# Performance work log

Measured on AMD Instinct MI355X. Metric: run time of the kernel, lower is better.

Reference implementation:

```python
import jax, jax.numpy as jnp
import numpy as np

B, IN, H = 131072, 128, 128


def setup_inputs() -> dict:
    key = jax.random.key(0)
    ks = jax.random.split(key, 8)
    scale_W = 1.0 / np.sqrt(IN + H)
    scale_r = 1.0 / np.sqrt(H)
    return {
        "x": jax.random.normal(ks[0], (B, IN), jnp.float32),
        "h": jax.random.normal(ks[1], (B, H), jnp.float32),
        "c": jax.random.normal(ks[2], (B, H), jnp.float32),
        "n": jax.random.uniform(ks[3], (B, H), jnp.float32, 0.1, 1.0),
        "m": jax.random.normal(ks[4], (B, H), jnp.float32),
        "W": jax.random.normal(ks[5], (IN + H, 4 * H), jnp.float32) * scale_W,
        "r": jax.random.normal(ks[6], (H, 4 * H), jnp.float32) * scale_r,
        "b": jnp.zeros((4 * H,), jnp.float32),
    }


def reference(x, h, c, n, m, W, r, b):
    # fused gate pre-activations: [B, 4H]
    combined = jnp.concatenate((x, h), axis=1)
    gates = combined @ W + h @ r + b
    i_raw, f_raw, z_raw, o_raw = jnp.split(gates, 4, axis=1)
    i = jnp.exp(i_raw)
    f = jax.nn.sigmoid(f_raw)
    z = jnp.tanh(z_raw)
    o = jax.nn.sigmoid(o_raw)
    # log-domain stabilizer (max trick), faithful to source incl. m overwrite
    m_new = jnp.maximum(jnp.log(f) + m, jnp.log(i))
    i_prime = jnp.exp(jnp.log(i) - m_new)
    f_prime = jnp.exp(jnp.log(f) + m_new - m_new)  # == f, as in source
    c_new = f_prime * c + i_prime * z
    n_new = f_prime * n + i_prime
    h_tilde = c_new / n_new
    h_new = o * jnp.tanh(h_tilde)
    return (h_new, c_new, n_new, m_new)
```

## Files before the change

kernel.cpp:

```cpp
#include <hip/hip_runtime.h>
#include <cstdint>

#define NROWS 131072
#define HD    128
#define NDIM  512
#define OUTQ  16777216

using bf16x8 = __attribute__((ext_vector_type(8))) short;
using f32x4  = __attribute__((ext_vector_type(4))) float;

#define SB() __builtin_amdgcn_sched_barrier(0)

__device__ __forceinline__ uint32_t bf16rne(float f) {
  uint32_t u = __builtin_bit_cast(uint32_t, f);
  return (u + 0x7fffu + ((u >> 16) & 1u)) >> 16;
}

__device__ __forceinline__ float tanhf_fast(float v) {
  float a = __builtin_fabsf(v);
  float e = __expf(-2.0f * a);
  float t = (1.0f - e) * __builtin_amdgcn_rcpf(1.0f + e);
  return v < 0.0f ? -t : t;
}

__device__ __forceinline__ f32x4 ldv(const float* p) {
  return *reinterpret_cast<const f32x4*>(p);
}

#define ASYNC16(g, l)                                                        \
  __builtin_amdgcn_global_load_lds(                                          \
      (const __attribute__((address_space(1))) void*)(g),                    \
      (__attribute__((address_space(3))) void*)(l), 16, 0, 0)

__global__ __launch_bounds__(256) void pack_weights(
    const float* __restrict__ W, const float* __restrict__ r,
    uint16_t* __restrict__ Bp) {
  int idx = blockIdx.x * 256 + threadIdx.x;
  int l  = idx & 63;
  int ts = idx >> 6;
  int s  = ts & 7;
  int t  = ts >> 3;
  int g  = t >> 3;
  int u  = t & 7;
  int t2 = u >> 1;
  int p  = u & 1;
  int m  = l & 15;
  int ncol  = g * 128 + t2 * 32 + ((m >> 2) << 3) + p * 4 + (m & 3);
  int kbase = s * 32 + ((l >> 4) << 3);
  uint32_t w[4];
#pragma unroll
  for (int jj = 0; jj < 4; ++jj) {
    int k0 = kbase + 2 * jj;
    float v0 = W[k0 * NDIM + ncol];
    float v1 = W[(k0 + 1) * NDIM + ncol];
    if (k0 >= 128)     v0 += r[(k0 - 128) * NDIM + ncol];
    if (k0 + 1 >= 128) v1 += r[(k0 + 1 - 128) * NDIM + ncol];
    w[jj] = bf16rne(v0) | (bf16rne(v1) << 16);
  }
  reinterpret_cast<uint4*>(Bp)[idx] = make_uint4(w[0], w[1], w[2], w[3]);
}

__global__ __launch_bounds__(256, 2) void slstm_fused(
    const float* __restrict__ x,  const float* __restrict__ h,
    const float* __restrict__ cs, const float* __restrict__ ns,
    const float* __restrict__ ms, const float* __restrict__ bias,
    const uint16_t* __restrict__ Bp, float* __restrict__ out) {
  __shared__ __align__(16) char smem[65536];
  const int tid  = threadIdx.x;
  const int wave = tid >> 6;
  const int lane = tid & 63;
  const int row0 = blockIdx.x * 64;
  const int l15  = lane & 15;
  const int lg   = lane >> 4;

  const int    myrow = row0 + wave * 16 + l15;
  const size_t rbase = (size_t)myrow * HD;
  const int    jb8   = lg * 8;
  const int    rl    = wave * 16 + l15;

  const char* wBytes = (const char*)Bp;
#define DMA_HALFSTEP(u)                                                      \
  {                                                                          \
    const char* gsrc = wBytes + (((size_t)(wave * 8 + (u)) * 8) << 10) + (lane << 4); \
    char* ldst = smem + (wave << 13);                                        \
    _Pragma("unroll")                                                        \
    for (int k = 0; k < 8; ++k)                                              \
      ASYNC16(gsrc + (k << 10), ldst + (k << 10));                           \
  }

  f32x4 cvA = ldv(cs + rbase + jb8), cvHiA = ldv(cs + rbase + jb8 + 4);
  f32x4 nvA = ldv(ns + rbase + jb8), nvHiA = ldv(ns + rbase + jb8 + 4);
  f32x4 mvA = ldv(ms + rbase + jb8), mvHiA = ldv(ms + rbase + jb8 + 4);

  DMA_HALFSTEP(0)

  bf16x8 a[8];
#pragma unroll
  for (int s = 0; s < 8; ++s) {
    const float* src = (s < 4 ? x : h) + rbase + ((s & 3) * 32 + lg * 8);
    f32x4 v0 = ldv(src);
    f32x4 v1 = ldv(src + 4);
    bf16x8 pk;
    pk[0] = (short)bf16rne(v0[0]);
    pk[1] = (short)bf16rne(v0[1]);
    pk[2] = (short)bf16rne(v0[2]);
    pk[3] = (short)bf16rne(v0[3]);
    pk[4] = (short)bf16rne(v1[0]);
    pk[5] = (short)bf16rne(v1[1]);
    pk[6] = (short)bf16rne(v1[2]);
    pk[7] = (short)bf16rne(v1[3]);
    a[s] = pk;
  }
  __syncthreads();

#define MFMA_PHASE(AI, AF, AZ, AO)                                           \
  {                                                                          \
    _Pragma("unroll")                                                        \
    for (int s = 0; s < 8; ++s) {                                            \
      const int lo = lane << 4;                                              \
      bf16x8 wI = *reinterpret_cast<const bf16x8*>(smem + ((0 * 8 + s) << 10) + lo); \
      bf16x8 wF = *reinterpret_cast<const bf16x8*>(smem + ((1 * 8 + s) << 10) + lo); \
      bf16x8 wZ = *reinterpret_cast<const bf16x8*>(smem + ((2 * 8 + s) << 10) + lo); \
      bf16x8 wO = *reinterpret_cast<const bf16x8*>(smem + ((3 * 8 + s) << 10) + lo); \
      AI = __builtin_amdgcn_mfma_f32_16x16x32_bf16(wI, a[s], AI, 0, 0, 0);   \
      AF = __builtin_amdgcn_mfma_f32_16x16x32_bf16(wF, a[s], AF, 0, 0, 0);   \
      AZ = __builtin_amdgcn_mfma_f32_16x16x32_bf16(wZ, a[s], AZ, 0, 0, 0);   \
      AO = __builtin_amdgcn_mfma_f32_16x16x32_bf16(wO, a[s], AO, 0, 0, 0);   \
    }                                                                        \
  }

  char* sbuf = smem + 32768;

#pragma unroll
  for (int t2 = 0; t2 < 4; ++t2) {
    const int cb = t2 * 32 + jb8;

    const f32x4 cvLo = cvA,   cvHi = cvHiA;
    const f32x4 nvLo = nvA,   nvHi = nvHiA;
    const f32x4 mvLo = mvA,   mvHi = mvHiA;

    SB(); asm volatile("s_waitcnt vmcnt(8)" ::: "memory"); SB();
    __builtin_amdgcn_s_barrier(); SB();

    f32x4 accI0 = {0,0,0,0}, accF0 = {0,0,0,0}, accZ0 = {0,0,0,0}, accO0 = {0,0,0,0};
    MFMA_PHASE(accI0, accF0, accZ0, accO0)

    SB(); __builtin_amdgcn_s_barrier(); SB();
    DMA_HALFSTEP(2 * t2 + 1)
    SB();
    asm volatile("s_waitcnt vmcnt(0)" ::: "memory"); SB();
    __builtin_amdgcn_s_barrier(); SB();

    const f32x4 bIlo = ldv(bias + cb),        bIhi = ldv(bias + cb + 4);
    const f32x4 bFlo = ldv(bias + 128 + cb),  bFhi = ldv(bias + 128 + cb + 4);
    const f32x4 bZlo = ldv(bias + 256 + cb),  bZhi = ldv(bias + 256 + cb + 4);
    const f32x4 bOlo = ldv(bias + 384 + cb),  bOhi = ldv(bias + 384 + cb + 4);
    if (t2 < 3) {
      const size_t pp = rbase + (t2 + 1) * 32 + jb8;
      cvA = ldv(cs + pp); cvHiA = ldv(cs + pp + 4);
      nvA = ldv(ns + pp); nvHiA = ldv(ns + pp + 4);
      mvA = ldv(ms + pp); mvHiA = ldv(ms + pp + 4);
    }

    f32x4 accI1 = {0,0,0,0}, accF1 = {0,0,0,0}, accZ1 = {0,0,0,0}, accO1 = {0,0,0,0};
    MFMA_PHASE(accI1, accF1, accZ1, accO1)

    f32x4 hnLo, hnHi, cnLo, cnHi, nnLo, nnHi, mnLo, mnHi;
#pragma unroll
    for (int d = 0; d < 8; ++d) {
      const int pp = d >> 2, rr = d & 3;
      const float i_raw = (pp ? accI1[rr] : accI0[rr]) + (pp ? bIhi[rr] : bIlo[rr]);
      const float f_raw = (pp ? accF1[rr] : accF0[rr]) + (pp ? bFhi[rr] : bFlo[rr]);
      const float z_raw = (pp ? accZ1[rr] : accZ0[rr]) + (pp ? bZhi[rr] : bZlo[rr]);
      const float o_raw = (pp ? accO1[rr] : accO0[rr]) + (pp ? bOhi[rr] : bOlo[rr]);
      const float cV = pp ? cvHi[rr] : cvLo[rr];
      const float nV = pp ? nvHi[rr] : nvLo[rr];
      const float mV = pp ? mvHi[rr] : mvLo[rr];
      float ef  = __expf(-f_raw);
      float den = 1.0f + ef;
      float fg  = __builtin_amdgcn_rcpf(den);
      float lgf = -__logf(den);
      float mnv = fmaxf(lgf + mV, i_raw);
      float ip  = __expf(i_raw - mnv);
      float zt  = tanhf_fast(z_raw);
      float og  = __builtin_amdgcn_rcpf(1.0f + __expf(-o_raw));
      float cnv = fg * cV + ip * zt;
      float nnv = fg * nV + ip;
      float hnv = og * tanhf_fast(cnv * __builtin_amdgcn_rcpf(nnv));
      if (pp == 0) { hnLo[rr] = hnv; cnLo[rr] = cnv; nnLo[rr] = nnv; mnLo[rr] = mnv; }
      else         { hnHi[rr] = hnv; cnHi[rr] = cnv; nnHi[rr] = nnv; mnHi[rr] = mnv; }
    }

    {
      const int rb   = rl << 7;
      const int sw   = rl & 7;
      const int kLo  = (lg << 1);
      const int kHi  = (lg << 1) | 1;
      const int oLo  = rb + (((kLo) ^ sw) << 4);
      const int oHi  = rb + (((kHi) ^ sw) << 4);
      *reinterpret_cast<f32x4*>(sbuf + 0 * 8192 + oLo) = hnLo;
      *reinterpret_cast<f32x4*>(sbuf + 0 * 8192 + oHi) = hnHi;
      *reinterpret_cast<f32x4*>(sbuf + 1 * 8192 + oLo) = cnLo;
      *reinterpret_cast<f32x4*>(sbuf + 1 * 8192 + oHi) = cnHi;
      *reinterpret_cast<f32x4*>(sbuf + 2 * 8192 + oLo) = nnLo;
      *reinterpret_cast<f32x4*>(sbuf + 2 * 8192 + oHi) = nnHi;
      *reinterpret_cast<f32x4*>(sbuf + 3 * 8192 + oLo) = mnLo;
      *reinterpret_cast<f32x4*>(sbuf + 3 * 8192 + oHi) = mnHi;
    }
    SB(); asm volatile("s_waitcnt lgkmcnt(0)" ::: "memory"); SB();
    __builtin_amdgcn_s_barrier(); SB();

    if (t2 < 3) DMA_HALFSTEP(2 * t2 + 2)
    SB();

    {
      float* abase = out + (size_t)wave * OUTQ + (size_t)row0 * HD + t2 * 32;
      const char* sb = sbuf + (wave << 13);
#pragma unroll
      for (int i = 0; i < 8; ++i) {
        const int r  = i * 8 + (lane >> 3);
        const int k  = lane & 7;
        f32x4 v = *reinterpret_cast<const f32x4*>(
            sb + (r << 7) + (((k ^ (r & 7))) << 4));
        __builtin_nontemporal_store(
            v, reinterpret_cast<f32x4*>(abase + (size_t)r * HD + k * 4));
      }
    }
  }
#undef DMA_HALFSTEP
#undef MFMA_PHASE
}

extern "C" void kernel_launch(void* const* d_in, const int* in_sizes, int n_in,
                              void* d_out, int out_size, void* d_ws, size_t ws_size,
                              hipStream_t stream) {
  const float* x = (const float*)d_in[0];
  const float* h = (const float*)d_in[1];
  const float* c = (const float*)d_in[2];
  const float* n = (const float*)d_in[3];
  const float* m = (const float*)d_in[4];
  const float* W = (const float*)d_in[5];
  const float* r = (const float*)d_in[6];
  const float* b = (const float*)d_in[7];
  uint16_t* Bp = (uint16_t*)d_ws;

  pack_weights<<<64, 256, 0, stream>>>(W, r, Bp);
  slstm_fused<<<NROWS / 64, 256, 0, stream>>>(x, h, c, n, m, b, Bp, (float*)d_out);
}
```

Baseline: 131.1 us.

## Double-buffer weight halves in LDS and split output staging into two passes

Weight tiles for both MFMA halves of a step are now prefetched together into two separate 32KB LDS regions. This removes the mid-step barrier and the DMA wait between the two MFMA phases. To fit in LDS, output staging is cut to 16KB and done in two rounds (h/c, then n/m), which adds barriers and LDS round trips. LDS use grows from 64KB to 80KB per block, which may lower occupancy under the 2-blocks launch bound.

```diff
diff --git a/kernel.cpp b/kernel.cpp
--- a/kernel.cpp
+++ b/kernel.cpp
@@ -65,7 +65,7 @@
     const float* __restrict__ cs, const float* __restrict__ ns,
     const float* __restrict__ ms, const float* __restrict__ bias,
     const uint16_t* __restrict__ Bp, float* __restrict__ out) {
-  __shared__ __align__(16) char smem[65536];
+  __shared__ __align__(16) char smem[81920];
   const int tid  = threadIdx.x;
   const int wave = tid >> 6;
   const int lane = tid & 63;
@@ -79,10 +79,10 @@
   const int    rl    = wave * 16 + l15;
 
   const char* wBytes = (const char*)Bp;
-#define DMA_HALFSTEP(u)                                                      \
+#define DMA_HALF(u, base)                                                    \
   {                                                                          \
     const char* gsrc = wBytes + (((size_t)(wave * 8 + (u)) * 8) << 10) + (lane << 4); \
-    char* ldst = smem + (wave << 13);                                        \
+    char* ldst = smem + (base) + (wave << 13);                               \
     _Pragma("unroll")                                                        \
     for (int k = 0; k < 8; ++k)                                              \
       ASYNC16(gsrc + (k << 10), ldst + (k << 10));                           \
@@ -92,7 +92,8 @@
   f32x4 nvA = ldv(ns + rbase + jb8), nvHiA = ldv(ns + rbase + jb8 + 4);
   f32x4 mvA = ldv(ms + rbase + jb8), mvHiA = ldv(ms + rbase + jb8 + 4);
 
-  DMA_HALFSTEP(0)
+  DMA_HALF(0, 0)
+  DMA_HALF(1, 32768)
 
   bf16x8 a[8];
 #pragma unroll
@@ -113,15 +114,15 @@
   }
   __syncthreads();
 
-#define MFMA_PHASE(AI, AF, AZ, AO)                                           \
+#define MFMA_PHASE(base, AI, AF, AZ, AO)                                     \
   {                                                                          \
     _Pragma("unroll")                                                        \
     for (int s = 0; s < 8; ++s) {                                            \
       const int lo = lane << 4;                                              \
-      bf16x8 wI = *reinterpret_cast<const bf16x8*>(smem + ((0 * 8 + s) << 10) + lo); \
-      bf16x8 wF = *reinterpret_cast<const bf16x8*>(smem + ((1 * 8 + s) << 10) + lo); \
-      bf16x8 wZ = *reinterpret_cast<const bf16x8*>(smem + ((2 * 8 + s) << 10) + lo); \
-      bf16x8 wO = *reinterpret_cast<const bf16x8*>(smem + ((3 * 8 + s) << 10) + lo); \
+      bf16x8 wI = *reinterpret_cast<const bf16x8*>(smem + (base) + ((0 * 8 + s) << 10) + lo); \
+      bf16x8 wF = *reinterpret_cast<const bf16x8*>(smem + (base) + ((1 * 8 + s) << 10) + lo); \
+      bf16x8 wZ = *reinterpret_cast<const bf16x8*>(smem + (base) + ((2 * 8 + s) << 10) + lo); \
+      bf16x8 wO = *reinterpret_cast<const bf16x8*>(smem + (base) + ((3 * 8 + s) << 10) + lo); \
       AI = __builtin_amdgcn_mfma_f32_16x16x32_bf16(wI, a[s], AI, 0, 0, 0);   \
       AF = __builtin_amdgcn_mfma_f32_16x16x32_bf16(wF, a[s], AF, 0, 0, 0);   \
       AZ = __builtin_amdgcn_mfma_f32_16x16x32_bf16(wZ, a[s], AZ, 0, 0, 0);   \
@@ -129,7 +130,7 @@
     }                                                                        \
   }
 
-  char* sbuf = smem + 32768;
+  char* sbuf = smem + 65536;
 
 #pragma unroll
   for (int t2 = 0; t2 < 4; ++t2) {
@@ -139,16 +140,13 @@
     const f32x4 nvLo = nvA,   nvHi = nvHiA;
     const f32x4 mvLo = mvA,   mvHi = mvHiA;
 
+    SB(); asm volatile("s_waitcnt vmcnt(16)" ::: "memory"); SB();
+    __builtin_amdgcn_s_barrier(); SB();
+
+    f32x4 accI0 = {0,0,0,0}, accF0 = {0,0,0,0}, accZ0 = {0,0,0,0}, accO0 = {0,0,0,0};
+    MFMA_PHASE(0, accI0, accF0, accZ0, accO0)
+
     SB(); asm volatile("s_waitcnt vmcnt(8)" ::: "memory"); SB();
-    __builtin_amdgcn_s_barrier(); SB();
-
-    f32x4 accI0 = {0,0,0,0}, accF0 = {0,0,0,0}, accZ0 = {0,0,0,0}, accO0 = {0,0,0,0};
-    MFMA_PHASE(accI0, accF0, accZ0, accO0)
-
-    SB(); __builtin_amdgcn_s_barrier(); SB();
-    DMA_HALFSTEP(2 * t2 + 1)
-    SB();
-    asm volatile("s_waitcnt vmcnt(0)" ::: "memory"); SB();
     __builtin_amdgcn_s_barrier(); SB();
 
     const f32x4 bIlo = ldv(bias + cb),        bIhi = ldv(bias + cb + 4);
@@ -163,7 +161,7 @@
     }
 
     f32x4 accI1 = {0,0,0,0}, accF1 = {0,0,0,0}, accZ1 = {0,0,0,0}, accO1 = {0,0,0,0};
-    MFMA_PHASE(accI1, accF1, accZ1, accO1)
+    MFMA_PHASE(32768, accI1, accF1, accZ1, accO1)
 
     f32x4 hnLo, hnHi, cnLo, cnHi, nnLo, nnHi, mnLo, mnHi;
 #pragma unroll
@@ -191,43 +189,66 @@
       else         { hnHi[rr] = hnv; cnHi[rr] = cnv; nnHi[rr] = nnv; mnHi[rr] = mnv; }
     }
 
+    const int rb   = rl << 7;
+    const int sw   = rl & 7;
+    const int oLo  = rb + ((((lg << 1)    ) ^ sw) << 4);
+    const int oHi  = rb + ((((lg << 1) | 1) ^ sw) << 4);
+
+    *reinterpret_cast<f32x4*>(sbuf + 0    + oLo) = hnLo;
+    *reinterpret_cast<f32x4*>(sbuf + 0    + oHi) = hnHi;
+    *reinterpret_cast<f32x4*>(sbuf + 8192 + oLo) = cnLo;
+    *reinterpret_cast<f32x4*>(sbuf + 8192 + oHi) = cnHi;
+    SB(); asm volatile("s_waitcnt lgkmcnt(0)" ::: "memory"); SB();
+    __builtin_amdgcn_s_barrier(); SB();
+
+    if (t2 < 3) {
+      DMA_HALF(2 * t2 + 2, 0)
+      DMA_HALF(2 * t2 + 3, 32768)
+    }
+    SB();
+
     {
-      const int rb   = rl << 7;
-      const int sw   = rl & 7;
-      const int kLo  = (lg << 1);
-      const int kHi  = (lg << 1) | 1;
-      const int oLo  = rb + (((kLo) ^ sw) << 4);
-      const int oHi  = rb + (((kHi) ^ sw) << 4);
-      *reinterpret_cast<f32x4*>(sbuf + 0 * 8192 + oLo) = hnLo;
-      *reinterpret_cast<f32x4*>(sbuf + 0 * 8192 + oHi) = hnHi;
-      *reinterpret_cast<f32x4*>(sbuf + 1 * 8192 + oLo) = cnLo;
-      *reinterpret_cast<f32x4*>(sbuf + 1 * 8192 + oHi) = cnHi;
-      *reinterpret_cast<f32x4*>(sbuf + 2 * 8192 + oLo) = nnLo;
-      *reinterpret_cast<f32x4*>(sbuf + 2 * 8192 + oHi) = nnHi;
-      *reinterpret_cast<f32x4*>(sbuf + 3 * 8192 + oLo) = mnLo;
-      *reinterpret_cast<f32x4*>(sbuf + 3 * 8192 + oHi) = mnHi;
-    }
-    SB(); asm volatile("s_waitcnt lgkmcnt(0)" ::: "memory"); SB();
-    __builtin_amdgcn_s_barrier(); SB();
-
-    if (t2 < 3) DMA_HALFSTEP(2 * t2 + 2)
-    SB();
-
-    {
-      float* abase = out + (size_t)wave * OUTQ + (size_t)row0 * HD + t2 * 32;
-      const char* sb = sbuf + (wave << 13);
-#pragma unroll
-      for (int i = 0; i < 8; ++i) {
-        const int r  = i * 8 + (lane >> 3);
-        const int k  = lane & 7;
+      const int aw  = wave >> 1;
+      const int rrb = (wave & 1) * 32;
+      const char* sb = sbuf + aw * 8192;
+      float* abase = out + (size_t)aw * OUTQ + (size_t)row0 * HD + t2 * 32;
+#pragma unroll
+      for (int i = 0; i < 4; ++i) {
+        const int r = rrb + i * 8 + (lane >> 3);
+        const int k = lane & 7;
         f32x4 v = *reinterpret_cast<const f32x4*>(
             sb + (r << 7) + (((k ^ (r & 7))) << 4));
         __builtin_nontemporal_store(
             v, reinterpret_cast<f32x4*>(abase + (size_t)r * HD + k * 4));
       }
     }
-  }
-#undef DMA_HALFSTEP
+    SB(); asm volatile("s_waitcnt lgkmcnt(0)" ::: "memory"); SB();
+    __builtin_amdgcn_s_barrier(); SB();
+
+    *reinterpret_cast<f32x4*>(sbuf + 0    + oLo) = nnLo;
+    *reinterpret_cast<f32x4*>(sbuf + 0    + oHi) = nnHi;
+    *reinterpret_cast<f32x4*>(sbuf + 8192 + oLo) = mnLo;
+    *reinterpret_cast<f32x4*>(sbuf + 8192 + oHi) = mnHi;
+    SB(); asm volatile("s_waitcnt lgkmcnt(0)" ::: "memory"); SB();
+    __builtin_amdgcn_s_barrier(); SB();
+
+    {
+      const int aw  = wave >> 1;
+      const int rrb = (wave & 1) * 32;
+      const char* sb = sbuf + aw * 8192;
+      float* abase = out + (size_t)(2 + aw) * OUTQ + (size_t)row0 * HD + t2 * 32;
+#pragma unroll
+      for (int i = 0; i < 4; ++i) {
+        const int r = rrb + i * 8 + (lane >> 3);
+        const int k = lane & 7;
+        f32x4 v = *reinterpret_cast<const f32x4*>(
+            sb + (r << 7) + (((k ^ (r & 7))) << 4));
+        __builtin_nontemporal_store(
+            v, reinterpret_cast<f32x4*>(abase + (size_t)r * HD + k * 4));
+      }
+    }
+  }
+#undef DMA_HALF
 #undef MFMA_PHASE
 }
 
```

New measurement: 130.4 us (median of 3 runs). Within noise of the previous version (-0.5%).
